# Performance work log

Measured on AMD Instinct MI355X. Metric: run time of the kernel, lower is better.

The kernel has to match this reference:

```python
import jax, jax.numpy as jnp
import numpy as np

MIN_NORM = 1e-15
EPS = 1e-7  # artanh domain clamp for fp32


def _tan_k(u, k):
    sk = jnp.sqrt(-k)
    return jnp.tanh(jnp.clip(sk * u, -15.0, 15.0)) / sk


def _artan_k(u, k):
    sk = jnp.sqrt(-k)
    return jnp.arctanh(jnp.clip(sk * u, -1.0 + EPS, 1.0 - EPS)) / sk


def _norm(x):
    return jnp.maximum(jnp.linalg.norm(x, axis=-1, keepdims=True), MIN_NORM)


def mobius_add(x, y, k):
    x2 = jnp.sum(x * x, axis=-1, keepdims=True)
    y2 = jnp.sum(y * y, axis=-1, keepdims=True)
    xy = jnp.sum(x * y, axis=-1, keepdims=True)
    num = (1.0 - 2.0 * k * xy - k * y2) * x + (1.0 + k * x2) * y
    den = 1.0 - 2.0 * k * xy + k * k * x2 * y2
    return num / jnp.maximum(den, MIN_NORM)


def mobius_matvec(M, x, k):
    # x: [..., d_in], M: [d_out, d_in]
    xn = _norm(x)
    mx = x @ M.T
    mxn = _norm(mx)
    res = _tan_k(mxn / xn * _artan_k(xn, k), k) * (mx / mxn)
    return jnp.where(jnp.all(mx == 0.0, axis=-1, keepdims=True), 0.0, res)


def mobius_pointwise_mul(w, x, k):
    xn = _norm(x)
    wx = w * x
    wxn = _norm(wx)
    res = _tan_k(wxn / xn * _artan_k(xn, k), k) * (wx / wxn)
    return jnp.where(jnp.all(wx == 0.0, axis=-1, keepdims=True), 0.0, res)


def expmap0(u, k):
    un = _norm(u)
    return _tan_k(un, k) * u / un


def logmap0(y, k):
    yn = _norm(y)
    return _artan_k(yn, k) * y / yn


def one_rnn_transform(W, h, U, x, b, k):
    Wh = mobius_matvec(W, h, k)
    Ux = mobius_matvec(U, x, k)
    return mobius_add(mobius_add(Wh, Ux, k), b, k)


def mobius_gru_cell(x, hx, w_ih, w_hh, b, k):
    W_ir, W_ih_, W_iz = jnp.split(w_ih, 3, axis=0)
    W_hr, W_hh_, W_hz = jnp.split(w_hh, 3, axis=0)
    b_r, b_h, b_z = b[0], b[1], b[2]
    z_t = jax.nn.sigmoid(logmap0(one_rnn_transform(W_hz, hx, W_iz, x, b_z, k), k))
    r_t = jax.nn.sigmoid(logmap0(one_rnn_transform(W_hr, hx, W_ir, x, b_r, k), k))
    rh_t = mobius_pointwise_mul(r_t, hx, k)
    h_tilde = one_rnn_transform(W_hh_, rh_t, W_ih_, x, b_h, k)
    delta_h = mobius_add(-hx, h_tilde, k)
    return mobius_add(hx, mobius_pointwise_mul(z_t, delta_h, k), k)


def mobius_gru_layer(x_tbd, h0, w_ih, w_hh, b, k, hyperbolic_input):
    # x_tbd: [T, B, D]; h0: [B, H]
    if not hyperbolic_input:
        x_tbd = expmap0(x_tbd, k)

    def step(hx, xt):
        h = expmap0(hx, k)
        h = mobius_gru_cell(xt, h, w_ih, w_hh, b, k)
        h = logmap0(h, k)
        return h, h

    h_last, outs = jax.lax.scan(step, h0, x_tbd)
    return outs, h_last  # outs: [T, B, H]


def setup_inputs() -> dict:
    key = jax.random.key(0)
    ks = jax.random.split(key, 8)
    B, T, D, H = 64, 1024, 256, 256
    stdv = 1.0 / np.sqrt(H)
    x = 0.02 * jax.random.normal(ks[0], (B, T, D), dtype=jnp.float32)
    k = jnp.float32(-1.0)  # hyperbolic curvature (geoopt sign convention)
    h0 = jnp.zeros((2, B, H), dtype=jnp.float32)
    w_ih0 = jax.random.uniform(ks[1], (3 * H, D), jnp.float32, -stdv, stdv)
    w_hh0 = jax.random.uniform(ks[2], (3 * H, H), jnp.float32, -stdv, stdv)
    b0 = 1e-5 * jax.random.normal(ks[3], (3, H), dtype=jnp.float32)
    w_ih1 = jax.random.uniform(ks[4], (3 * H, H), jnp.float32, -stdv, stdv)
    w_hh1 = jax.random.uniform(ks[5], (3 * H, H), jnp.float32, -stdv, stdv)
    b1 = 1e-5 * jax.random.normal(ks[6], (3, H), dtype=jnp.float32)
    return {"x": x, "k": k, "h0": h0, "w_ih0": w_ih0, "w_hh0": w_hh0, "b0": b0,
            "w_ih1": w_ih1, "w_hh1": w_hh1, "b1": b1}


def reference(x, k, h0, w_ih0, w_hh0, b0, w_ih1, w_hh1, b1):
    # x: [B, T, D]; source unbinds dim 1 as time -> scan over time-major.
    xt = jnp.swapaxes(x, 0, 1)  # [T, B, D]
    out0, hl0 = mobius_gru_layer(xt, h0[0], w_ih0, w_hh0, b0, k, hyperbolic_input=False)
    out1, hl1 = mobius_gru_layer(out0, h0[1], w_ih1, w_hh1, b1, k, hyperbolic_input=True)
    ht = jnp.stack([hl0, hl1])  # [num_layers, B, H]
    return out1, ht
```

## Files before the change

kernel.cpp:

```cpp
#include <hip/hip_runtime.h>
#include <cstdint>
#include <cstddef>

#define MINN 1e-15f
#define EPSA 1e-7f
#define C_L2E 1.44269504088896341f
#define C_LN2 0.69314718055994531f

typedef _Float16 half_t;
typedef _Float16 half2_t __attribute__((ext_vector_type(2)));

#if defined(__has_builtin)
#if __has_builtin(__builtin_amdgcn_update_dpp) && __has_builtin(__builtin_amdgcn_readlane)
#define USE_DPP 1
#endif
#endif

__device__ __forceinline__ float fexp2_(float x) {
#if defined(__has_builtin) && __has_builtin(__builtin_amdgcn_exp2f)
    return __builtin_amdgcn_exp2f(x);
#else
    return exp2f(x);
#endif
}
__device__ __forceinline__ float flog2_(float x) {
#if defined(__has_builtin) && __has_builtin(__builtin_amdgcn_logf)
    return __builtin_amdgcn_logf(x);
#else
    return log2f(x);
#endif
}
__device__ __forceinline__ float frcp_(float x) {
#if defined(__has_builtin) && __has_builtin(__builtin_amdgcn_rcpf)
    return __builtin_amdgcn_rcpf(x);
#else
    return 1.f / x;
#endif
}
__device__ __forceinline__ float tan_k_(float u, float sk, float rsk) {
    float a = fminf(fmaxf(sk * u, -15.f), 15.f);
    float t = fexp2_(a * (2.f * C_L2E));
    return (1.f - 2.f * frcp_(t + 1.f)) * rsk;
}
__device__ __forceinline__ float artan_k_(float u, float sk, float rsk) {
    float a = fminf(fmaxf(sk * u, -1.f + EPSA), 1.f - EPSA);
    return flog2_((1.f + a) * frcp_(1.f - a)) * (0.5f * C_LN2) * rsk;
}
__device__ __forceinline__ float sigm_(float x) {
    return frcp_(1.f + fexp2_(-x * C_L2E));
}
__device__ __forceinline__ float wave_sum(float v) {
#pragma unroll
    for (int off = 32; off; off >>= 1) v += __shfl_xor(v, off, 64);
    return v;
}

#ifdef USE_DPP
template <int CTRL, int RM, int BM>
__device__ __forceinline__ float dppmov_(float x) {
    return __builtin_bit_cast(float,
        __builtin_amdgcn_update_dpp(0, __builtin_bit_cast(int, x), CTRL, RM, BM, false));
}
#endif
__device__ __forceinline__ float wsum63_(float x) {
#ifdef USE_DPP
    x += dppmov_<0x111, 0xf, 0xf>(x);
    x += dppmov_<0x112, 0xf, 0xf>(x);
    x += dppmov_<0x114, 0xf, 0xe>(x);
    x += dppmov_<0x118, 0xf, 0xc>(x);
    x += dppmov_<0x142, 0xa, 0xf>(x);
    x += dppmov_<0x143, 0xc, 0xf>(x);
    return x;
#else
    return wave_sum(x);
#endif
}
__device__ __forceinline__ float gsum8_(float x) {
#ifdef USE_DPP
    x += dppmov_<0x111, 0xf, 0xf>(x);
    x += dppmov_<0x112, 0xf, 0xf>(x);
    x += dppmov_<0x114, 0xf, 0xe>(x);
    return x;
#else
    x += __shfl_xor(x, 1, 64);
    x += __shfl_xor(x, 2, 64);
    x += __shfl_xor(x, 4, 64);
    return x;
#endif
}
__device__ __forceinline__ float rdlane_(float x, int l) {
#ifdef USE_DPP
    return __builtin_bit_cast(float,
        __builtin_amdgcn_readlane(__builtin_bit_cast(int, x), l));
#else
    return __shfl(x, l, 64);
#endif
}
template <int N>
__device__ __forceinline__ void bredX(float* v, float* redbuf, int tid) {
    const int lane = tid & 63, wave = tid >> 6;
#pragma unroll
    for (int n = 0; n < N; ++n) {
        float s = wsum63_(v[n]);
        if (lane == 63) redbuf[n * 8 + wave] = s;
    }
    __syncthreads();
    float part = redbuf[lane & (8 * N - 1)];
    part = gsum8_(part);
#pragma unroll
    for (int n = 0; n < N; ++n) v[n] = rdlane_(part, 8 * n + 7);
}

__device__ __forceinline__ float dot2acc(uint32_t w, uint32_t h, float acc) {
#if defined(__has_builtin) && __has_builtin(__builtin_amdgcn_fdot2)
    return __builtin_amdgcn_fdot2(__builtin_bit_cast(half2_t, w),
                                  __builtin_bit_cast(half2_t, h), acc, false);
#else
    half2_t a = __builtin_bit_cast(half2_t, w);
    half2_t b = __builtin_bit_cast(half2_t, h);
    acc = fmaf((float)a[0], (float)b[0], acc);
    return fmaf((float)a[1], (float)b[1], acc);
#endif
}

__global__ __launch_bounds__(256) void kt_transpose(
    const float* __restrict__ a0, const float* __restrict__ a1,
    float* __restrict__ o0, float* __restrict__ o1) {
    int idx = blockIdx.x * 256 + threadIdx.x;
    int m = idx / 196608, rem = idx % 196608;
    int j = rem >> 8, kk = rem & 255;
    const float* in = (m == 0) ? a0 : a1;
    float* outp     = (m == 0) ? o0 : o1;
    outp[kk * 768 + j] = in[j * 256 + kk];
}

__global__ __launch_bounds__(256) void kt_prep1(
    const float* __restrict__ whh0, const float* __restrict__ whh1,
    uint32_t* __restrict__ p0, uint32_t* __restrict__ p1) {
    int idx = blockIdx.x * 256 + threadIdx.x;
    int l = idx >> 16, e = idx & 65535;
    int r4 = e >> 11, rem = e & 2047;
    int t = rem >> 2, m = r4 * 4 + (rem & 3);
    int lane = t & 63, wave = t >> 6;
    int p = wave * 32 + (lane & 31), ph = lane >> 5;
    int g = m >> 6, mi = m & 63;
    int row = g ? (512 + p) : p;
    int i = ph * 128 + 2 * mi;
    const float* w = l ? whh1 : whh0;
    half2_t hv;
    hv[0] = (half_t)w[row * 256 + i];
    hv[1] = (half_t)w[row * 256 + i + 1];
    (l ? p1 : p0)[e] = __builtin_bit_cast(uint32_t, hv);
}

__global__ __launch_bounds__(256) void kt_prep2(
    const float* __restrict__ whh0, const float* __restrict__ whh1,
    uint32_t* __restrict__ p0, uint32_t* __restrict__ p1) {
    int idx = blockIdx.x * 256 + threadIdx.x;
    int l = idx >> 15, e = idx & 32767;
    int i2 = e >> 8, j = e & 255;
    const float* w = l ? whh1 : whh0;
    half2_t hv;
    hv[0] = (half_t)w[(256 + j) * 256 + 2 * i2];
    hv[1] = (half_t)w[(256 + j) * 256 + 2 * i2 + 1];
    (l ? p1 : p0)[e] = __builtin_bit_cast(uint32_t, hv);
}

__global__ __launch_bounds__(256) void kt_init(
    const float* __restrict__ h0, float* __restrict__ hcar) {
    int i = blockIdx.x * 256 + threadIdx.x;
    hcar[i] = h0[i];
}
__global__ __launch_bounds__(256) void kt_final(
    const float* __restrict__ hcar, float* __restrict__ dst) {
    int i = blockIdx.x * 256 + threadIdx.x;
    dst[i] = hcar[i];
}

__global__ __launch_bounds__(256) void kt_gemm(
    const float* __restrict__ A, long long strideB,
    const float* __restrict__ Bt, float* __restrict__ C,
    float* __restrict__ ax_arr, const float* __restrict__ kptr, int mode) {
    __shared__ float As[16][68];
    __shared__ float Bs[16][68];
    __shared__ float sS[64];
    int tid = threadIdx.x;
    int row0 = blockIdx.y * 64, col0 = blockIdx.x * 64;

    {
        float kk = kptr[0], sk = sqrtf(-kk), rsk = frcp_(sk);
        int row = tid >> 2, q = tid & 3;
        int rc = row0 + row;
        size_t base = (size_t)(rc >> 6) * strideB + (size_t)(rc & 63) * 256 + q * 64;
        float n2 = 0.f;
#pragma unroll
        for (int u = 0; u < 16; ++u) {
            float4 v = *(const float4*)&A[base + u * 4];
            n2 += v.x * v.x + v.y * v.y + v.z * v.z + v.w * v.w;
        }
        n2 += __shfl_xor(n2, 1, 64);
        n2 += __shfl_xor(n2, 2, 64);
        float n = sqrtf(n2);
        float s, xn;
        if (mode == 0) {
            float nrm = fmaxf(n, MINN);
            float tk = tan_k_(nrm, sk, rsk);
            s = tk * frcp_(nrm);
            xn = fmaxf(tk * (n * frcp_(nrm)), MINN);
        } else {
            s = 1.f;
            xn = fmaxf(n, MINN);
        }
        float ax = artan_k_(xn, sk, rsk) * frcp_(xn);
        if (q == 0) { sS[row] = s; ax_arr[rc] = ax; }
    }

    int ty = tid >> 4, tx = tid & 15;
    int ra = tid >> 2, kq = tid & 3;
    int kb = tid >> 4, cq = tid & 15;
    float acc[4][4] = {};
    __syncthreads();
#pragma unroll 1
    for (int kt = 0; kt < 16; ++kt) {
        int k0 = kt * 16;
        int rc = row0 + ra;
        size_t aoff = (size_t)(rc >> 6) * strideB + (size_t)(rc & 63) * 256 + k0 + kq * 4;
        float4 av = *(const float4*)&A[aoff];
        float sc = sS[ra];
        float4 bv = *(const float4*)&Bt[(size_t)(k0 + kb) * 768 + col0 + cq * 4];
        As[kq * 4 + 0][ra] = av.x * sc;
        As[kq * 4 + 1][ra] = av.y * sc;
        As[kq * 4 + 2][ra] = av.z * sc;
        As[kq * 4 + 3][ra] = av.w * sc;
        *(float4*)&Bs[kb][cq * 4] = bv;
        __syncthreads();
#pragma unroll
        for (int kk = 0; kk < 16; ++kk) {
            float4 a4 = *(const float4*)&As[kk][ty * 4];
            float4 b4 = *(const float4*)&Bs[kk][tx * 4];
            float aa[4] = {a4.x, a4.y, a4.z, a4.w};
            float bb[4] = {b4.x, b4.y, b4.z, b4.w};
#pragma unroll
            for (int i = 0; i < 4; ++i)
#pragma unroll
                for (int j = 0; j < 4; ++j)
                    acc[i][j] = fmaf(aa[i], bb[j], acc[i][j]);
        }
        __syncthreads();
    }
#pragma unroll
    for (int i = 0; i < 4; ++i) {
        size_t row = (size_t)row0 + ty * 4 + i;
        *(float4*)&C[row * 768 + col0 + tx * 4] =
            make_float4(acc[i][0], acc[i][1], acc[i][2], acc[i][3]);
    }
}

__global__ __launch_bounds__(256) void kt_mscale(
    float* __restrict__ mx, const float* __restrict__ ax_arr,
    float* __restrict__ uxn, float* __restrict__ uxb,
    const float* __restrict__ bias, const float* __restrict__ kptr) {
    int lane = threadIdx.x & 63;
    int p = blockIdx.x * 4 + (threadIdx.x >> 6);
    int r = p / 3;
    int g = p - r * 3;
    float k = kptr[0], sk = sqrtf(-k), rsk = frcp_(sk);
    float* ptr = mx + (size_t)r * 768 + g * 256 + lane * 4;
    float4 v = *(const float4*)ptr;
    float4 b4 = *(const float4*)&bias[g * 256 + lane * 4];
    float n2 = wave_sum(v.x * v.x + v.y * v.y + v.z * v.z + v.w * v.w);
    float vb = wave_sum(v.x * b4.x + v.y * b4.y + v.z * b4.z + v.w * b4.w);
    float nt = sqrtf(n2);
    float mxn = fmaxf(nt, MINN);
    float arg = mxn * ax_arr[r];
    float tk = tan_k_(arg, sk, rsk);
    float f = tk * frcp_(mxn);
    v.x *= f; v.y *= f; v.z *= f; v.w *= f;
    *(float4*)ptr = v;
    if (lane == 0) { uxn[p] = tk * (nt * frcp_(mxn)); uxb[p] = f * vb; }
}

__global__ __launch_bounds__(512, 1) void kt_scan2(
    const float* __restrict__ Ux_0, const float* __restrict__ uxn_0,
    const float* __restrict__ uxb_0,
    const uint32_t* __restrict__ w1pk_0, const uint32_t* __restrict__ whh2g_0,
    const float* __restrict__ bias_0, float* __restrict__ hcar_0,
    float* __restrict__ out_0, long long sb_0, long long st_0,
    const float* __restrict__ Ux_1, const float* __restrict__ uxn_1,
    const float* __restrict__ uxb_1,
    const uint32_t* __restrict__ w1pk_1, const uint32_t* __restrict__ whh2g_1,
    const float* __restrict__ bias_1, float* __restrict__ hcar_1,
    float* __restrict__ out_1, long long sb_1, long long st_1,
    const float* __restrict__ kptr, int Tc, int nrole0) {
    __shared__ uint4 whhS[8192];
    __shared__ uint32_t hy2S[128];
    __shared__ uint32_t rh2S[128];
    __shared__ float redbuf[2][64];

    const int tid = threadIdx.x;
    const int role = (blockIdx.x >= nrole0) ? 1 : 0;
    const int bb = role ? (int)blockIdx.x - nrole0 : (int)blockIdx.x;

    const float* Ux      = role ? Ux_1 : Ux_0;
    const float* uxn     = role ? uxn_1 : uxn_0;
    const float* uxb     = role ? uxb_1 : uxb_0;
    const uint32_t* w1pk = role ? w1pk_1 : w1pk_0;
    const uint32_t* whh2g= role ? whh2g_1 : whh2g_0;
    const float* bias    = role ? bias_1 : bias_0;
    float* hcar          = role ? hcar_1 : hcar_0;
    float* outbase       = role ? out_1 : out_0;
    const long long stride_b = role ? sb_1 : sb_0;
    const long long stride_t = role ? st_1 : st_0;

    const int lane = tid & 63, wave = tid >> 6;
    const int p = wave * 32 + (lane & 31), ph = lane >> 5;
    const float k = kptr[0], sk = sqrtf(-k), rsk = frcp_(sk);

    for (int idx = tid; idx < 32768; idx += 512) {
        uint32_t v = whh2g[idx];
        int i2 = idx >> 8, col = idx & 255;
        ((uint32_t*)whhS)[((i2 >> 2) * 256 + col) * 4 + (i2 & 3)] = v;
    }
    uint32_t w1[128];
    {
        const uint4* wp = (const uint4*)w1pk;
#pragma unroll
        for (int r4 = 0; r4 < 32; ++r4) {
            uint4 v = wp[r4 * 512 + tid];
            w1[4 * r4 + 0] = v.x; w1[4 * r4 + 1] = v.y;
            w1[4 * r4 + 2] = v.z; w1[4 * r4 + 3] = v.w;
        }
    }

    const float br = bias[p], bh = bias[256 + p], bz = bias[512 + p];
    float h = hcar[bb * 256 + p];
    __syncthreads();
    float v4[4] = {br * br, bh * bh, bz * bz, h * h};
    bredX<4>(v4, redbuf[0], tid);
    const float bn2r = 0.5f * v4[0], bn2h = 0.5f * v4[1], bn2z = 0.5f * v4[2];
    float S_h2 = 0.5f * v4[3];

    float* myout = outbase + (size_t)bb * stride_b;
    const float* uxpb = Ux + (size_t)bb * Tc * 768;
    const float* unpb = uxn + (size_t)bb * Tc * 3;
    const float* ubpb = uxb + (size_t)bb * Tc * 3;

    float puxr = uxpb[p], puxh = uxpb[256 + p], puxz = uxpb[512 + p];
    float punr = unpb[0], punh = unpb[1], punz = unpb[2];
    float pubr = ubpb[0], pubh = ubpb[1], pubz = ubpb[2];

    for (int t = 0; t < Tc; ++t) {
        const float uxr = puxr, uxh = puxh, uxz = puxz;
        const float unr = punr, unh = punh, unz = punz;
        const float S_ubr = pubr, S_ubh = pubh, S_ubz = pubz;

        float hn = sqrtf(S_h2);
        float nrm = fmaxf(hn, MINN);
        float tk0 = tan_k_(nrm, sk, rsk);
        float chy = tk0 * frcp_(nrm);
        float hy = chy * h;
        float Shy2 = chy * chy * S_h2;
        float xnh = fmaxf(tk0 * (hn * frcp_(nrm)), MINN);
        float axh = artan_k_(xnh, sk, rsk) * frcp_(xnh);
        if (ph == 0) ((half_t*)hy2S)[p] = (half_t)hy;
        __syncthreads();

        if (t + 1 < Tc) {
            const float* uxp2 = uxpb + (size_t)(t + 1) * 768;
            puxr = uxp2[p]; puxh = uxp2[256 + p]; puxz = uxp2[512 + p];
            const float* unp2 = unpb + (size_t)(t + 1) * 3;
            punr = unp2[0]; punh = unp2[1]; punz = unp2[2];
            const float* ubp2 = ubpb + (size_t)(t + 1) * 3;
            pubr = ubp2[0]; pubh = ubp2[1]; pubz = ubp2[2];
        }

        float prA[4] = {0.f, 0.f, 0.f, 0.f};
        float pzA[4] = {0.f, 0.f, 0.f, 0.f};
        {
            const uint4* hp = (const uint4*)hy2S + ph * 16;
#pragma unroll
            for (int c4 = 0; c4 < 4; ++c4) {
                uint32_t hv[16];
#pragma unroll
                for (int u = 0; u < 4; ++u) {
                    uint4 v = hp[c4 * 4 + u];
                    hv[4 * u + 0] = v.x; hv[4 * u + 1] = v.y;
                    hv[4 * u + 2] = v.z; hv[4 * u + 3] = v.w;
                }
#pragma unroll
                for (int m = 0; m < 16; ++m) {
                    prA[c4] = dot2acc(w1[c4 * 16 + m], hv[m], prA[c4]);
                    pzA[c4] = dot2acc(w1[64 + c4 * 16 + m], hv[m], pzA[c4]);
                }
            }
        }
        float pr = (prA[0] + prA[1]) + (prA[2] + prA[3]);
        float pz = (pzA[0] + pzA[1]) + (pzA[2] + pzA[3]);
        const float mr = pr + __shfl_xor(pr, 32, 64);
        const float mz = pz + __shfl_xor(pz, 32, 64);

        float vr[8] = {mr * mr, mz * mz, mr * uxr, mz * uxz,
                       mr * br, mz * bz, h * uxh, h * bh};
        bredX<8>(vr, redbuf[0], tid);
        const float S_mr2 = 0.5f * vr[0], S_mz2 = 0.5f * vr[1];
        const float S_mru = 0.5f * vr[2], S_mzu = 0.5f * vr[3];
        const float S_mrb = 0.5f * vr[4], S_mzb = 0.5f * vr[5];
        const float S_huxh = 0.5f * vr[6], S_hbh = 0.5f * vr[7];

        const float m_   = ph ? mz    : mr;
        const float S2_  = ph ? S_mz2 : S_mr2;
        const float Su_  = ph ? S_mzu : S_mru;
        const float Sb_  = ph ? S_mzb : S_mrb;
        const float Sub_ = ph ? S_ubz : S_ubr;
        const float bn2_ = ph ? bn2z  : bn2r;
        const float un_  = ph ? unz   : unr;
        const float ux_  = ph ? uxz   : uxr;
        const float b_   = ph ? bz    : br;
        float g_own;
        {
            float mxn = fmaxf(sqrtf(S2_), MINN);
            float tk = tan_k_(mxn * axh, sk, rsk);
            float f = tk * frcp_(mxn);
            float x2 = f * f * S2_, y2 = un_ * un_, xy = f * Su_;
            float a = 1.f - 2.f * k * xy - k * y2;
            float bq = 1.f + k * x2;
            float rd = frcp_(fmaxf(1.f - 2.f * k * xy + k * k * x2 * y2, MINN));
            float c1 = (a * f * m_ + bq * ux_) * rd;
            float Sc12 = (a * a * x2 + 2.f * a * bq * xy + bq * bq * y2) * (rd * rd);
            float Sc1b = (a * f * Sb_ + bq * Sub_) * rd;
            float g = 1.f - 2.f * k * Sc1b - k * bn2_;
            float dl = 1.f + k * Sc12;
            float re = frcp_(fmaxf(1.f - 2.f * k * Sc1b + k * k * Sc12 * bn2_, MINN));
            float c2 = (g * c1 + dl * b_) * re;
            float Sc22 = (g * g * Sc12 + 2.f * g * dl * Sc1b + dl * dl * bn2_) * (re * re);
            float yn = fmaxf(sqrtf(Sc22), MINN);
            float lg = artan_k_(yn, sk, rsk) * frcp_(yn) * c2;
            g_own = sigm_(lg);
        }
        const float g_oth = __shfl_xor(g_own, 32, 64);
        const float r_t = ph ? g_oth : g_own;
        const float z_t = ph ? g_own : g_oth;

        float wx = r_t * hy;
        if (ph == 0) ((half_t*)rh2S)[p] = (half_t)wx;
        {
            float s1v = wsum63_(wx * wx);
            if (lane == 63) redbuf[1][wave] = s1v;
        }
        __syncthreads();

        float part1 = gsum8_(redbuf[1][lane & 7]);
        const float S_wx2 = 0.5f * rdlane_(part1, 7);
        float wxt = sqrtf(S_wx2);
        float wxn = fmaxf(wxt, MINN);
        float tkw = tan_k_(wxn * axh, sk, rsk);
        float fw = tkw * frcp_(wxn);
        float rhn = tkw * (wxt * frcp_(wxn));

        float qA[4] = {0.f, 0.f, 0.f, 0.f};
        {
            const uint4* rp = (const uint4*)rh2S + ph * 16;
#pragma unroll
            for (int u = 0; u < 16; ++u) {
                uint4 wv = whhS[(ph * 16 + u) * 256 + p];
                uint4 rv = rp[u];
                int s = u >> 2;
                qA[s] = dot2acc(wv.x, rv.x, qA[s]);
                qA[s] = dot2acc(wv.y, rv.y, qA[s]);
                qA[s] = dot2acc(wv.z, rv.z, qA[s]);
                qA[s] = dot2acc(wv.w, rv.w, qA[s]);
            }
        }
        float qq = (qA[0] + qA[1]) + (qA[2] + qA[3]);
        const float mh = fw * (qq + __shfl_xor(qq, 32, 64));

        float v4b[4] = {mh * mh, mh * uxh, mh * bh, hy * mh};
        bredX<4>(v4b, redbuf[0], tid);
        const float S_mh2 = 0.5f * v4b[0], S_mhu = 0.5f * v4b[1];
        const float S_mhb = 0.5f * v4b[2], S_hymh = 0.5f * v4b[3];

        float wz, Sdelta2;
        {
            float xnrh = fmaxf(rhn, MINN);
            float axrh = artan_k_(xnrh, sk, rsk) * frcp_(xnrh);
            float mxn = fmaxf(sqrtf(S_mh2), MINN);
            float tk = tan_k_(mxn * axrh, sk, rsk);
            float f = tk * frcp_(mxn);
            float x2 = f * f * S_mh2, y2 = unh * unh, xy = f * S_mhu;
            float a = 1.f - 2.f * k * xy - k * y2;
            float bq = 1.f + k * x2;
            float rd = frcp_(fmaxf(1.f - 2.f * k * xy + k * k * x2 * y2, MINN));
            float c1 = (a * f * mh + bq * uxh) * rd;
            float Sc12 = (a * a * x2 + 2.f * a * bq * xy + bq * bq * y2) * (rd * rd);
            float Sc1b = (a * f * S_mhb + bq * S_ubh) * rd;
            float S_hyc1 = (a * f * S_hymh + bq * chy * S_huxh) * rd;
            float g = 1.f - 2.f * k * Sc1b - k * bn2h;
            float dl = 1.f + k * Sc12;
            float re = frcp_(fmaxf(1.f - 2.f * k * Sc1b + k * k * Sc12 * bn2h, MINN));
            float htl = (g * c1 + dl * bh) * re;
            float Shtl2 = (g * g * Sc12 + 2.f * g * dl * Sc1b + dl * dl * bn2h) * (re * re);
            float S_hyhtl = (g * S_hyc1 + dl * chy * S_hbh) * re;
            float ad = 1.f + 2.f * k * S_hyhtl - k * Shtl2;
            float bd = 1.f + k * Shy2;
            float rdd = frcp_(fmaxf(1.f + 2.f * k * S_hyhtl + k * k * Shy2 * Shtl2, MINN));
            float delta = (ad * (-hy) + bd * htl) * rdd;
            Sdelta2 = (ad * ad * Shy2 - 2.f * ad * bd * S_hyhtl + bd * bd * Shtl2) * (rdd * rdd);
            wz = z_t * delta;
        }
        float v2[2] = {wz * wz, hy * wz};
        bredX<2>(v2, redbuf[1], tid);
        const float S_wz2 = 0.5f * v2[0], S_hywz = 0.5f * v2[1];

        {
            float dnc = fmaxf(sqrtf(Sdelta2), MINN);
            float axd = artan_k_(dnc, sk, rsk) * frcp_(dnc);
            float wzt = sqrtf(S_wz2);
            float wznc = fmaxf(wzt, MINN);
            float tkzd = tan_k_(wznc * axd, sk, rsk);
            float fz = tkzd * frcp_(wznc);
            float zd = fz * wz;
            float zdn2 = fz * fz * S_wz2;
            float S_hyzd = fz * S_hywz;
            float an = 1.f - 2.f * k * S_hyzd - k * zdn2;
            float bn_ = 1.f + k * Shy2;
            float rdn = frcp_(fmaxf(1.f - 2.f * k * S_hyzd + k * k * Shy2 * zdn2, MINN));
            float hnew = (an * hy + bn_ * zd) * rdn;
            float Shnew2 = (an * an * Shy2 + 2.f * an * bn_ * S_hyzd + bn_ * bn_ * zdn2) * (rdn * rdn);
            float yn = fmaxf(sqrtf(Shnew2), MINN);
            float ayn = artan_k_(yn, sk, rsk) * frcp_(yn);
            float outv = ayn * hnew;
            if (ph == 0) myout[(size_t)t * stride_t + p] = outv;
            h = outv;
            S_h2 = ayn * ayn * Shnew2;
        }
    }
    if (ph == 0) hcar[bb * 256 + p] = h;
}

extern "C" void kernel_launch(void* const* d_in, const int* in_sizes, int n_in,
                              void* d_out, int out_size, void* d_ws, size_t ws_size,
                              hipStream_t stream) {
    const float* x    = (const float*)d_in[0];
    const float* kptr = (const float*)d_in[1];
    const float* h0   = (const float*)d_in[2];
    const float* wih0 = (const float*)d_in[3];
    const float* whh0 = (const float*)d_in[4];
    const float* b0   = (const float*)d_in[5];
    const float* wih1 = (const float*)d_in[6];
    const float* whh1 = (const float*)d_in[7];
    const float* b1   = (const float*)d_in[8];
    float* out = (float*)d_out;
    float* ws  = (float*)d_ws;

    const int B = 64, T = 1024, H = 256;
    const int CT = 64, NC = 16;
    const int RC = B * CT;

    float* wt_ih0 = ws;
    float* wt_ih1 = wt_ih0 + 196608;
    uint32_t* w1pk0  = (uint32_t*)(wt_ih1 + 196608);
    uint32_t* w1pk1  = w1pk0 + 65536;
    uint32_t* whh2g0 = w1pk1 + 65536;
    uint32_t* whh2g1 = whh2g0 + 32768;
    float* hcar  = (float*)(whh2g1 + 32768);
    float* ax0   = hcar + 32768;
    float* ax1   = ax0 + RC;
    float* uxn0  = ax1 + RC;
    float* uxn1  = uxn0 + 3 * RC;
    float* uxb0  = uxn1 + 3 * RC;
    float* uxb1  = uxb0 + 3 * RC;
    float* out0c = uxb1 + 3 * RC;
    float* mx0   = out0c + (size_t)RC * H;
    float* mx1   = mx0 + (size_t)RC * 768;

    float* hcar0 = hcar;
    float* hcar1 = hcar + (size_t)B * H;

    dim3 blk(256);
    kt_transpose<<<dim3(1536), blk, 0, stream>>>(wih0, wih1, wt_ih0, wt_ih1);
    kt_prep1<<<dim3(512), blk, 0, stream>>>(whh0, whh1, w1pk0, w1pk1);
    kt_prep2<<<dim3(256), blk, 0, stream>>>(whh0, whh1, whh2g0, whh2g1);
    kt_init<<<dim3(128), blk, 0, stream>>>(h0, hcar);

    const long long sbx = (long long)T * 256;
    const long long sbc = (long long)CT * 256;

    {
        const float* xc = x;
        kt_gemm<<<dim3(12, RC / 64), blk, 0, stream>>>(xc, sbx, wt_ih0, mx0, ax0, kptr, 0);
        kt_mscale<<<dim3(RC * 3 / 4), blk, 0, stream>>>(mx0, ax0, uxn0, uxb0, b0, kptr);
        kt_scan2<<<dim3(B), dim3(512), 0, stream>>>(
            mx0, uxn0, uxb0, w1pk0, whh2g0, b0, hcar0, out0c, sbc, 256LL,
            mx0, uxn0, uxb0, w1pk0, whh2g0, b0, hcar0, out0c, sbc, 256LL,
            kptr, CT, B);
    }
    for (int c = 1; c < NC; ++c) {
        const float* xc = x + (size_t)c * CT * 256;
        kt_gemm<<<dim3(12, RC / 64), blk, 0, stream>>>(xc, sbx, wt_ih0, mx0, ax0, kptr, 0);
        kt_mscale<<<dim3(RC * 3 / 4), blk, 0, stream>>>(mx0, ax0, uxn0, uxb0, b0, kptr);
        kt_gemm<<<dim3(12, RC / 64), blk, 0, stream>>>(out0c, sbc, wt_ih1, mx1, ax1, kptr, 1);
        kt_mscale<<<dim3(RC * 3 / 4), blk, 0, stream>>>(mx1, ax1, uxn1, uxb1, b1, kptr);
        kt_scan2<<<dim3(2 * B), dim3(512), 0, stream>>>(
            mx0, uxn0, uxb0, w1pk0, whh2g0, b0, hcar0, out0c, sbc, 256LL,
            mx1, uxn1, uxb1, w1pk1, whh2g1, b1, hcar1,
            out + (size_t)(c - 1) * CT * B * H, 256LL, (long long)B * H,
            kptr, CT, B);
    }
    {
        kt_gemm<<<dim3(12, RC / 64), blk, 0, stream>>>(out0c, sbc, wt_ih1, mx1, ax1, kptr, 1);
        kt_mscale<<<dim3(RC * 3 / 4), blk, 0, stream>>>(mx1, ax1, uxn1, uxb1, b1, kptr);
        kt_scan2<<<dim3(B), dim3(512), 0, stream>>>(
            mx1, uxn1, uxb1, w1pk1, whh2g1, b1, hcar1,
            out + (size_t)(NC - 1) * CT * B * H, 256LL, (long long)B * H,
            mx1, uxn1, uxb1, w1pk1, whh2g1, b1, hcar1,
            out + (size_t)(NC - 1) * CT * B * H, 256LL, (long long)B * H,
            kptr, CT, B);
    }
    kt_final<<<dim3(128), blk, 0, stream>>>(hcar, out + (size_t)T * B * H);
}
```

Before: 6.134 ms.

## Fuse GEMM, scaling and scan into one pipelined mega-kernel with double buffering

After: 5.367 ms. -12.5%, faster.

```diff
diff --git a/kernel.cpp b/kernel.cpp
--- a/kernel.cpp
+++ b/kernel.cpp
@@ -177,149 +177,145 @@
     dst[i] = hcar[i];
 }
 
-__global__ __launch_bounds__(256) void kt_gemm(
-    const float* __restrict__ A, long long strideB,
-    const float* __restrict__ Bt, float* __restrict__ C,
-    float* __restrict__ ax_arr, const float* __restrict__ kptr, int mode) {
-    __shared__ float As[16][68];
-    __shared__ float Bs[16][68];
-    __shared__ float sS[64];
-    int tid = threadIdx.x;
-    int row0 = blockIdx.y * 64, col0 = blockIdx.x * 64;
-
-    {
-        float kk = kptr[0], sk = sqrtf(-kk), rsk = frcp_(sk);
-        int row = tid >> 2, q = tid & 3;
-        int rc = row0 + row;
-        size_t base = (size_t)(rc >> 6) * strideB + (size_t)(rc & 63) * 256 + q * 64;
-        float n2 = 0.f;
-#pragma unroll
-        for (int u = 0; u < 16; ++u) {
-            float4 v = *(const float4*)&A[base + u * 4];
-            n2 += v.x * v.x + v.y * v.y + v.z * v.z + v.w * v.w;
-        }
-        n2 += __shfl_xor(n2, 1, 64);
-        n2 += __shfl_xor(n2, 2, 64);
-        float n = sqrtf(n2);
-        float s, xn;
-        if (mode == 0) {
-            float nrm = fmaxf(n, MINN);
-            float tk = tan_k_(nrm, sk, rsk);
-            s = tk * frcp_(nrm);
-            xn = fmaxf(tk * (n * frcp_(nrm)), MINN);
-        } else {
-            s = 1.f;
-            xn = fmaxf(n, MINN);
-        }
-        float ax = artan_k_(xn, sk, rsk) * frcp_(xn);
-        if (q == 0) { sS[row] = s; ax_arr[rc] = ax; }
-    }
-
-    int ty = tid >> 4, tx = tid & 15;
-    int ra = tid >> 2, kq = tid & 3;
-    int kb = tid >> 4, cq = tid & 15;
-    float acc[4][4] = {};
-    __syncthreads();
+struct MegaArgs {
+    const float* s_mx[2]; const float* s_ax[2];
+    const uint32_t* s_w1[2]; const uint32_t* s_whh[2];
+    const float* s_bias[2]; float* s_hcar[2]; float* s_out[2];
+    long long s_sb[2]; long long s_st[2];
+    const float* g_A[2]; long long g_sB[2]; const float* g_Bt[2];
+    float* g_C[2]; float* g_ax[2]; int g_mode[2];
+    int nscan; int ngemm; int Tc;
+    const float* kptr;
+};
+
+__global__ __launch_bounds__(512, 1) void kt_mega(MegaArgs a) {
+    union Smem {
+        struct {
+            uint4 whhS[8192];
+            uint32_t hy2S[128];
+            uint32_t rh2S[128];
+            float redbuf[2][64];
+            float4 fS4[32];
+            float4 unS4[32];
+            float4 ubS4[32];
+        } s;
+        struct {
+            float As[16][68];
+            float Bs[16][132];
+            float sS[64];
+        } g;
+    };
+    __shared__ Smem sm;
+    const int tid = threadIdx.x;
+    const int bid = blockIdx.x;
+    const float k = a.kptr[0];
+    const float sk = sqrtf(-k), rsk = frcp_(sk);
+    const int Tc = a.Tc;
+
+    if (bid >= a.nscan * 64) {
+        int gb = bid - a.nscan * 64;
+        int gs = gb / 192, w = gb % 192;
+        const float* A = a.g_A[gs];
+        const long long strideB = a.g_sB[gs];
+        const float* Bt = a.g_Bt[gs];
+        float* C = a.g_C[gs];
+        float* axo = a.g_ax[gs];
+        const int mode = a.g_mode[gs];
+        int rb = w / 6, cb = w % 6;
+        int row0 = rb * 64, col0 = cb * 128;
+
+        {
+            int row = tid >> 3, oct = tid & 7;
+            int rc = row0 + row;
+            size_t base = (size_t)(rc >> 5) * strideB + (size_t)(rc & 31) * 256 + oct * 32;
+            float n2 = 0.f;
+#pragma unroll
+            for (int u = 0; u < 8; ++u) {
+                float4 v = *(const float4*)&A[base + u * 4];
+                n2 += v.x * v.x + v.y * v.y + v.z * v.z + v.w * v.w;
+            }
+            n2 += __shfl_xor(n2, 1, 64);
+            n2 += __shfl_xor(n2, 2, 64);
+            n2 += __shfl_xor(n2, 4, 64);
+            float n = sqrtf(n2);
+            float s, xn;
+            if (mode == 0) {
+                float nrm = fmaxf(n, MINN);
+                float tk = tan_k_(nrm, sk, rsk);
+                s = tk * frcp_(nrm);
+                xn = fmaxf(tk * (n * frcp_(nrm)), MINN);
+            } else {
+                s = 1.f;
+                xn = fmaxf(n, MINN);
+            }
+            float ax = artan_k_(xn, sk, rsk) * frcp_(xn);
+            if (oct == 0) { sm.g.sS[row] = s; if (cb == 0) axo[rc] = ax; }
+        }
+        __syncthreads();
+
+        int ty = tid >> 5, tx = tid & 31;
+        float acc[4][4] = {};
 #pragma unroll 1
-    for (int kt = 0; kt < 16; ++kt) {
-        int k0 = kt * 16;
-        int rc = row0 + ra;
-        size_t aoff = (size_t)(rc >> 6) * strideB + (size_t)(rc & 63) * 256 + k0 + kq * 4;
-        float4 av = *(const float4*)&A[aoff];
-        float sc = sS[ra];
-        float4 bv = *(const float4*)&Bt[(size_t)(k0 + kb) * 768 + col0 + cq * 4];
-        As[kq * 4 + 0][ra] = av.x * sc;
-        As[kq * 4 + 1][ra] = av.y * sc;
-        As[kq * 4 + 2][ra] = av.z * sc;
-        As[kq * 4 + 3][ra] = av.w * sc;
-        *(float4*)&Bs[kb][cq * 4] = bv;
-        __syncthreads();
-#pragma unroll
-        for (int kk = 0; kk < 16; ++kk) {
-            float4 a4 = *(const float4*)&As[kk][ty * 4];
-            float4 b4 = *(const float4*)&Bs[kk][tx * 4];
-            float aa[4] = {a4.x, a4.y, a4.z, a4.w};
-            float bb[4] = {b4.x, b4.y, b4.z, b4.w};
-#pragma unroll
-            for (int i = 0; i < 4; ++i)
-#pragma unroll
-                for (int j = 0; j < 4; ++j)
-                    acc[i][j] = fmaf(aa[i], bb[j], acc[i][j]);
-        }
-        __syncthreads();
-    }
-#pragma unroll
-    for (int i = 0; i < 4; ++i) {
-        size_t row = (size_t)row0 + ty * 4 + i;
-        *(float4*)&C[row * 768 + col0 + tx * 4] =
-            make_float4(acc[i][0], acc[i][1], acc[i][2], acc[i][3]);
-    }
-}
-
-__global__ __launch_bounds__(256) void kt_mscale(
-    float* __restrict__ mx, const float* __restrict__ ax_arr,
-    float* __restrict__ uxn, float* __restrict__ uxb,
-    const float* __restrict__ bias, const float* __restrict__ kptr) {
-    int lane = threadIdx.x & 63;
-    int p = blockIdx.x * 4 + (threadIdx.x >> 6);
-    int r = p / 3;
-    int g = p - r * 3;
-    float k = kptr[0], sk = sqrtf(-k), rsk = frcp_(sk);
-    float* ptr = mx + (size_t)r * 768 + g * 256 + lane * 4;
-    float4 v = *(const float4*)ptr;
-    float4 b4 = *(const float4*)&bias[g * 256 + lane * 4];
-    float n2 = wave_sum(v.x * v.x + v.y * v.y + v.z * v.z + v.w * v.w);
-    float vb = wave_sum(v.x * b4.x + v.y * b4.y + v.z * b4.z + v.w * b4.w);
-    float nt = sqrtf(n2);
-    float mxn = fmaxf(nt, MINN);
-    float arg = mxn * ax_arr[r];
-    float tk = tan_k_(arg, sk, rsk);
-    float f = tk * frcp_(mxn);
-    v.x *= f; v.y *= f; v.z *= f; v.w *= f;
-    *(float4*)ptr = v;
-    if (lane == 0) { uxn[p] = tk * (nt * frcp_(mxn)); uxb[p] = f * vb; }
-}
-
-__global__ __launch_bounds__(512, 1) void kt_scan2(
-    const float* __restrict__ Ux_0, const float* __restrict__ uxn_0,
-    const float* __restrict__ uxb_0,
-    const uint32_t* __restrict__ w1pk_0, const uint32_t* __restrict__ whh2g_0,
-    const float* __restrict__ bias_0, float* __restrict__ hcar_0,
-    float* __restrict__ out_0, long long sb_0, long long st_0,
-    const float* __restrict__ Ux_1, const float* __restrict__ uxn_1,
-    const float* __restrict__ uxb_1,
-    const uint32_t* __restrict__ w1pk_1, const uint32_t* __restrict__ whh2g_1,
-    const float* __restrict__ bias_1, float* __restrict__ hcar_1,
-    float* __restrict__ out_1, long long sb_1, long long st_1,
-    const float* __restrict__ kptr, int Tc, int nrole0) {
-    __shared__ uint4 whhS[8192];
-    __shared__ uint32_t hy2S[128];
-    __shared__ uint32_t rh2S[128];
-    __shared__ float redbuf[2][64];
-
-    const int tid = threadIdx.x;
-    const int role = (blockIdx.x >= nrole0) ? 1 : 0;
-    const int bb = role ? (int)blockIdx.x - nrole0 : (int)blockIdx.x;
-
-    const float* Ux      = role ? Ux_1 : Ux_0;
-    const float* uxn     = role ? uxn_1 : uxn_0;
-    const float* uxb     = role ? uxb_1 : uxb_0;
-    const uint32_t* w1pk = role ? w1pk_1 : w1pk_0;
-    const uint32_t* whh2g= role ? whh2g_1 : whh2g_0;
-    const float* bias    = role ? bias_1 : bias_0;
-    float* hcar          = role ? hcar_1 : hcar_0;
-    float* outbase       = role ? out_1 : out_0;
-    const long long stride_b = role ? sb_1 : sb_0;
-    const long long stride_t = role ? st_1 : st_0;
+        for (int kt = 0; kt < 16; ++kt) {
+            int k0 = kt * 16;
+            if (tid < 256) {
+                int ra = tid >> 2, kq = tid & 3;
+                int rc = row0 + ra;
+                size_t aoff = (size_t)(rc >> 5) * strideB + (size_t)(rc & 31) * 256 + k0 + kq * 4;
+                float4 av = *(const float4*)&A[aoff];
+                float sc = sm.g.sS[ra];
+                sm.g.As[kq * 4 + 0][ra] = av.x * sc;
+                sm.g.As[kq * 4 + 1][ra] = av.y * sc;
+                sm.g.As[kq * 4 + 2][ra] = av.z * sc;
+                sm.g.As[kq * 4 + 3][ra] = av.w * sc;
+            }
+            {
+                int kb = tid >> 5, cq = tid & 31;
+                float4 bv = *(const float4*)&Bt[(size_t)(k0 + kb) * 768 + col0 + cq * 4];
+                *(float4*)&sm.g.Bs[kb][cq * 4] = bv;
+            }
+            __syncthreads();
+#pragma unroll
+            for (int kk = 0; kk < 16; ++kk) {
+                float4 a4 = *(const float4*)&sm.g.As[kk][ty * 4];
+                float4 b4 = *(const float4*)&sm.g.Bs[kk][tx * 4];
+                float aa[4] = {a4.x, a4.y, a4.z, a4.w};
+                float bb[4] = {b4.x, b4.y, b4.z, b4.w};
+#pragma unroll
+                for (int i = 0; i < 4; ++i)
+#pragma unroll
+                    for (int j = 0; j < 4; ++j)
+                        acc[i][j] = fmaf(aa[i], bb[j], acc[i][j]);
+            }
+            __syncthreads();
+        }
+#pragma unroll
+        for (int i = 0; i < 4; ++i) {
+            size_t row = (size_t)row0 + ty * 4 + i;
+            *(float4*)&C[row * 768 + col0 + tx * 4] =
+                make_float4(acc[i][0], acc[i][1], acc[i][2], acc[i][3]);
+        }
+        return;
+    }
+
+    const int slot = bid >> 6, bb = bid & 63;
+    const float* mx      = a.s_mx[slot];
+    const float* axp     = a.s_ax[slot];
+    const uint32_t* w1pk = a.s_w1[slot];
+    const uint32_t* whh2g= a.s_whh[slot];
+    const float* bias    = a.s_bias[slot];
+    float* hcar          = a.s_hcar[slot];
+    float* outbase       = a.s_out[slot];
+    const long long stride_b = a.s_sb[slot];
+    const long long stride_t = a.s_st[slot];
 
     const int lane = tid & 63, wave = tid >> 6;
     const int p = wave * 32 + (lane & 31), ph = lane >> 5;
-    const float k = kptr[0], sk = sqrtf(-k), rsk = frcp_(sk);
 
     for (int idx = tid; idx < 32768; idx += 512) {
         uint32_t v = whh2g[idx];
         int i2 = idx >> 8, col = idx & 255;
-        ((uint32_t*)whhS)[((i2 >> 2) * 256 + col) * 4 + (i2 & 3)] = v;
+        ((uint32_t*)sm.s.whhS)[((i2 >> 2) * 256 + col) * 4 + (i2 & 3)] = v;
     }
     uint32_t w1[128];
     {
@@ -332,27 +328,51 @@
         }
     }
 
+    const float* uxpb = mx + (size_t)bb * Tc * 768;
+
+    {
+        const int UPW = (Tc * 3) >> 3;
+#pragma unroll 1
+        for (int i = 0; i < UPW; ++i) {
+            int u = wave * UPW + i;
+            int tt = u / 3, g = u - 3 * tt;
+            const float* rowp = uxpb + (size_t)tt * 768 + g * 256 + lane * 4;
+            float4 v = *(const float4*)rowp;
+            float4 b4 = *(const float4*)&bias[g * 256 + lane * 4];
+            float n2 = wsum63_(v.x * v.x + v.y * v.y + v.z * v.z + v.w * v.w);
+            float vb = wsum63_(v.x * b4.x + v.y * b4.y + v.z * b4.z + v.w * b4.w);
+            if (lane == 63) {
+                float nt = sqrtf(n2);
+                float mxn = fmaxf(nt, MINN);
+                float arg = mxn * axp[bb * Tc + tt];
+                float tk = tan_k_(arg, sk, rsk);
+                float f = tk * frcp_(mxn);
+                ((float*)&sm.s.fS4[tt])[g] = f;
+                ((float*)&sm.s.unS4[tt])[g] = tk * (nt * frcp_(mxn));
+                ((float*)&sm.s.ubS4[tt])[g] = f * vb;
+            }
+        }
+    }
+
     const float br = bias[p], bh = bias[256 + p], bz = bias[512 + p];
     float h = hcar[bb * 256 + p];
     __syncthreads();
     float v4[4] = {br * br, bh * bh, bz * bz, h * h};
-    bredX<4>(v4, redbuf[0], tid);
+    bredX<4>(v4, sm.s.redbuf[0], tid);
     const float bn2r = 0.5f * v4[0], bn2h = 0.5f * v4[1], bn2z = 0.5f * v4[2];
     float S_h2 = 0.5f * v4[3];
 
     float* myout = outbase + (size_t)bb * stride_b;
-    const float* uxpb = Ux + (size_t)bb * Tc * 768;
-    const float* unpb = uxn + (size_t)bb * Tc * 3;
-    const float* ubpb = uxb + (size_t)bb * Tc * 3;
-
-    float puxr = uxpb[p], puxh = uxpb[256 + p], puxz = uxpb[512 + p];
-    float punr = unpb[0], punh = unpb[1], punz = unpb[2];
-    float pubr = ubpb[0], pubh = ubpb[1], pubz = ubpb[2];
+
+    float prawr = uxpb[p], prawh = uxpb[256 + p], prawz = uxpb[512 + p];
 
     for (int t = 0; t < Tc; ++t) {
-        const float uxr = puxr, uxh = puxh, uxz = puxz;
-        const float unr = punr, unh = punh, unz = punz;
-        const float S_ubr = pubr, S_ubh = pubh, S_ubz = pubz;
+        const float4 ff = sm.s.fS4[t];
+        const float4 uu = sm.s.unS4[t];
+        const float4 ub = sm.s.ubS4[t];
+        const float uxr = prawr * ff.x, uxh = prawh * ff.y, uxz = prawz * ff.z;
+        const float unr = uu.x, unh = uu.y, unz = uu.z;
+        const float S_ubr = ub.x, S_ubh = ub.y, S_ubz = ub.z;
 
         float hn = sqrtf(S_h2);
         float nrm = fmaxf(hn, MINN);
@@ -362,22 +382,18 @@
         float Shy2 = chy * chy * S_h2;
         float xnh = fmaxf(tk0 * (hn * frcp_(nrm)), MINN);
         float axh = artan_k_(xnh, sk, rsk) * frcp_(xnh);
-        if (ph == 0) ((half_t*)hy2S)[p] = (half_t)hy;
+        if (ph == 0) ((half_t*)sm.s.hy2S)[p] = (half_t)hy;
         __syncthreads();
 
         if (t + 1 < Tc) {
             const float* uxp2 = uxpb + (size_t)(t + 1) * 768;
-            puxr = uxp2[p]; puxh = uxp2[256 + p]; puxz = uxp2[512 + p];
-            const float* unp2 = unpb + (size_t)(t + 1) * 3;
-            punr = unp2[0]; punh = unp2[1]; punz = unp2[2];
-            const float* ubp2 = ubpb + (size_t)(t + 1) * 3;
-            pubr = ubp2[0]; pubh = ubp2[1]; pubz = ubp2[2];
+            prawr = uxp2[p]; prawh = uxp2[256 + p]; prawz = uxp2[512 + p];
         }
 
         float prA[4] = {0.f, 0.f, 0.f, 0.f};
         float pzA[4] = {0.f, 0.f, 0.f, 0.f};
         {
-            const uint4* hp = (const uint4*)hy2S + ph * 16;
+            const uint4* hp = (const uint4*)sm.s.hy2S + ph * 16;
 #pragma unroll
             for (int c4 = 0; c4 < 4; ++c4) {
                 uint32_t hv[16];
@@ -401,7 +417,7 @@
 
         float vr[8] = {mr * mr, mz * mz, mr * uxr, mz * uxz,
                        mr * br, mz * bz, h * uxh, h * bh};
-        bredX<8>(vr, redbuf[0], tid);
+        bredX<8>(vr, sm.s.redbuf[0], tid);
         const float S_mr2 = 0.5f * vr[0], S_mz2 = 0.5f * vr[1];
         const float S_mru = 0.5f * vr[2], S_mzu = 0.5f * vr[3];
         const float S_mrb = 0.5f * vr[4], S_mzb = 0.5f * vr[5];
@@ -422,12 +438,12 @@
             float tk = tan_k_(mxn * axh, sk, rsk);
             float f = tk * frcp_(mxn);
             float x2 = f * f * S2_, y2 = un_ * un_, xy = f * Su_;
-            float a = 1.f - 2.f * k * xy - k * y2;
+            float aq = 1.f - 2.f * k * xy - k * y2;
             float bq = 1.f + k * x2;
             float rd = frcp_(fmaxf(1.f - 2.f * k * xy + k * k * x2 * y2, MINN));
-            float c1 = (a * f * m_ + bq * ux_) * rd;
-            float Sc12 = (a * a * x2 + 2.f * a * bq * xy + bq * bq * y2) * (rd * rd);
-            float Sc1b = (a * f * Sb_ + bq * Sub_) * rd;
+            float c1 = (aq * f * m_ + bq * ux_) * rd;
+            float Sc12 = (aq * aq * x2 + 2.f * aq * bq * xy + bq * bq * y2) * (rd * rd);
+            float Sc1b = (aq * f * Sb_ + bq * Sub_) * rd;
             float g = 1.f - 2.f * k * Sc1b - k * bn2_;
             float dl = 1.f + k * Sc12;
             float re = frcp_(fmaxf(1.f - 2.f * k * Sc1b + k * k * Sc12 * bn2_, MINN));
@@ -442,14 +458,14 @@
         const float z_t = ph ? g_own : g_oth;
 
         float wx = r_t * hy;
-        if (ph == 0) ((half_t*)rh2S)[p] = (half_t)wx;
+        if (ph == 0) ((half_t*)sm.s.rh2S)[p] = (half_t)wx;
         {
             float s1v = wsum63_(wx * wx);
-            if (lane == 63) redbuf[1][wave] = s1v;
+            if (lane == 63) sm.s.redbuf[1][wave] = s1v;
         }
         __syncthreads();
 
-        float part1 = gsum8_(redbuf[1][lane & 7]);
+        float part1 = gsum8_(sm.s.redbuf[1][lane & 7]);
         const float S_wx2 = 0.5f * rdlane_(part1, 7);
         float wxt = sqrtf(S_wx2);
         float wxn = fmaxf(wxt, MINN);
@@ -459,10 +475,10 @@
 
         float qA[4] = {0.f, 0.f, 0.f, 0.f};
         {
-            const uint4* rp = (const uint4*)rh2S + ph * 16;
+            const uint4* rp = (const uint4*)sm.s.rh2S + ph * 16;
 #pragma unroll
             for (int u = 0; u < 16; ++u) {
-                uint4 wv = whhS[(ph * 16 + u) * 256 + p];
+                uint4 wv = sm.s.whhS[(ph * 16 + u) * 256 + p];
                 uint4 rv = rp[u];
                 int s = u >> 2;
                 qA[s] = dot2acc(wv.x, rv.x, qA[s]);
@@ -475,7 +491,7 @@
         const float mh = fw * (qq + __shfl_xor(qq, 32, 64));
 
         float v4b[4] = {mh * mh, mh * uxh, mh * bh, hy * mh};
-        bredX<4>(v4b, redbuf[0], tid);
+        bredX<4>(v4b, sm.s.redbuf[0], tid);
         const float S_mh2 = 0.5f * v4b[0], S_mhu = 0.5f * v4b[1];
         const float S_mhb = 0.5f * v4b[2], S_hymh = 0.5f * v4b[3];
 
@@ -487,13 +503,13 @@
             float tk = tan_k_(mxn * axrh, sk, rsk);
             float f = tk * frcp_(mxn);
             float x2 = f * f * S_mh2, y2 = unh * unh, xy = f * S_mhu;
-            float a = 1.f - 2.f * k * xy - k * y2;
+            float aq = 1.f - 2.f * k * xy - k * y2;
             float bq = 1.f + k * x2;
             float rd = frcp_(fmaxf(1.f - 2.f * k * xy + k * k * x2 * y2, MINN));
-            float c1 = (a * f * mh + bq * uxh) * rd;
-            float Sc12 = (a * a * x2 + 2.f * a * bq * xy + bq * bq * y2) * (rd * rd);
-            float Sc1b = (a * f * S_mhb + bq * S_ubh) * rd;
-            float S_hyc1 = (a * f * S_hymh + bq * chy * S_huxh) * rd;
+            float c1 = (aq * f * mh + bq * uxh) * rd;
+            float Sc12 = (aq * aq * x2 + 2.f * aq * bq * xy + bq * bq * y2) * (rd * rd);
+            float Sc1b = (aq * f * S_mhb + bq * S_ubh) * rd;
+            float S_hyc1 = (aq * f * S_hymh + bq * chy * S_huxh) * rd;
             float g = 1.f - 2.f * k * Sc1b - k * bn2h;
             float dl = 1.f + k * Sc12;
             float re = frcp_(fmaxf(1.f - 2.f * k * Sc1b + k * k * Sc12 * bn2h, MINN));
@@ -508,7 +524,7 @@
             wz = z_t * delta;
         }
         float v2[2] = {wz * wz, hy * wz};
-        bredX<2>(v2, redbuf[1], tid);
+        bredX<2>(v2, sm.s.redbuf[1], tid);
         const float S_wz2 = 0.5f * v2[0], S_hywz = 0.5f * v2[1];
 
         {
@@ -553,8 +569,9 @@
     float* ws  = (float*)d_ws;
 
     const int B = 64, T = 1024, H = 256;
-    const int CT = 64, NC = 16;
+    const int CT = 32, NC = 32;
     const int RC = B * CT;
+    const int GBLK = (RC / 64) * 6;
 
     float* wt_ih0 = ws;
     float* wt_ih1 = wt_ih0 + 196608;
@@ -563,16 +580,20 @@
     uint32_t* whh2g0 = w1pk1 + 65536;
     uint32_t* whh2g1 = whh2g0 + 32768;
     float* hcar  = (float*)(whh2g1 + 32768);
-    float* ax0   = hcar + 32768;
-    float* ax1   = ax0 + RC;
-    float* uxn0  = ax1 + RC;
-    float* uxn1  = uxn0 + 3 * RC;
-    float* uxb0  = uxn1 + 3 * RC;
-    float* uxb1  = uxb0 + 3 * RC;
-    float* out0c = uxb1 + 3 * RC;
-    float* mx0   = out0c + (size_t)RC * H;
-    float* mx1   = mx0 + (size_t)RC * 768;
-
+    float* ax0b_[2], *ax1b_[2], *out0c_[2], *mx0_[2], *mx1_[2];
+    {
+        float* cur = hcar + 32768;
+        ax0b_[0] = cur; cur += RC;
+        ax0b_[1] = cur; cur += RC;
+        ax1b_[0] = cur; cur += RC;
+        ax1b_[1] = cur; cur += RC;
+        out0c_[0] = cur; cur += (size_t)RC * H;
+        out0c_[1] = cur; cur += (size_t)RC * H;
+        mx0_[0] = cur; cur += (size_t)RC * 768;
+        mx0_[1] = cur; cur += (size_t)RC * 768;
+        mx1_[0] = cur; cur += (size_t)RC * 768;
+        mx1_[1] = cur; cur += (size_t)RC * 768;
+    }
     float* hcar0 = hcar;
     float* hcar1 = hcar + (size_t)B * H;
 
@@ -582,39 +603,52 @@
     kt_prep2<<<dim3(256), blk, 0, stream>>>(whh0, whh1, whh2g0, whh2g1);
     kt_init<<<dim3(128), blk, 0, stream>>>(h0, hcar);
 
-    const long long sbx = (long long)T * 256;
-    const long long sbc = (long long)CT * 256;
-
     {
-        const float* xc = x;
-        kt_gemm<<<dim3(12, RC / 64), blk, 0, stream>>>(xc, sbx, wt_ih0, mx0, ax0, kptr, 0);
-        kt_mscale<<<dim3(RC * 3 / 4), blk, 0, stream>>>(mx0, ax0, uxn0, uxb0, b0, kptr);
-        kt_scan2<<<dim3(B), dim3(512), 0, stream>>>(
-            mx0, uxn0, uxb0, w1pk0, whh2g0, b0, hcar0, out0c, sbc, 256LL,
-            mx0, uxn0, uxb0, w1pk0, whh2g0, b0, hcar0, out0c, sbc, 256LL,
-            kptr, CT, B);
-    }
-    for (int c = 1; c < NC; ++c) {
-        const float* xc = x + (size_t)c * CT * 256;
-        kt_gemm<<<dim3(12, RC / 64), blk, 0, stream>>>(xc, sbx, wt_ih0, mx0, ax0, kptr, 0);
-        kt_mscale<<<dim3(RC * 3 / 4), blk, 0, stream>>>(mx0, ax0, uxn0, uxb0, b0, kptr);
-        kt_gemm<<<dim3(12, RC / 64), blk, 0, stream>>>(out0c, sbc, wt_ih1, mx1, ax1, kptr, 1);
-        kt_mscale<<<dim3(RC * 3 / 4), blk, 0, stream>>>(mx1, ax1, uxn1, uxb1, b1, kptr);
-        kt_scan2<<<dim3(2 * B), dim3(512), 0, stream>>>(
-            mx0, uxn0, uxb0, w1pk0, whh2g0, b0, hcar0, out0c, sbc, 256LL,
-            mx1, uxn1, uxb1, w1pk1, whh2g1, b1, hcar1,
-            out + (size_t)(c - 1) * CT * B * H, 256LL, (long long)B * H,
-            kptr, CT, B);
-    }
-    {
-        kt_gemm<<<dim3(12, RC / 64), blk, 0, stream>>>(out0c, sbc, wt_ih1, mx1, ax1, kptr, 1);
-        kt_mscale<<<dim3(RC * 3 / 4), blk, 0, stream>>>(mx1, ax1, uxn1, uxb1, b1, kptr);
-        kt_scan2<<<dim3(B), dim3(512), 0, stream>>>(
-            mx1, uxn1, uxb1, w1pk1, whh2g1, b1, hcar1,
-            out + (size_t)(NC - 1) * CT * B * H, 256LL, (long long)B * H,
-            mx1, uxn1, uxb1, w1pk1, whh2g1, b1, hcar1,
-            out + (size_t)(NC - 1) * CT * B * H, 256LL, (long long)B * H,
-            kptr, CT, B);
+        MegaArgs a{};
+        a.nscan = 0; a.ngemm = 1; a.Tc = CT; a.kptr = kptr;
+        a.g_A[0] = x; a.g_sB[0] = (long long)T * 256; a.g_Bt[0] = wt_ih0;
+        a.g_C[0] = mx0_[0]; a.g_ax[0] = ax0b_[0]; a.g_mode[0] = 0;
+        kt_mega<<<dim3(GBLK), dim3(512), 0, stream>>>(a);
+    }
+
+    for (int c = 0; c <= NC + 1; ++c) {
+        MegaArgs a{};
+        int ns = 0, ng = 0;
+        if (c <= NC - 1) {
+            a.s_mx[ns] = mx0_[c & 1]; a.s_ax[ns] = ax0b_[c & 1];
+            a.s_w1[ns] = w1pk0; a.s_whh[ns] = whh2g0;
+            a.s_bias[ns] = b0; a.s_hcar[ns] = hcar0;
+            a.s_out[ns] = out0c_[c & 1];
+            a.s_sb[ns] = (long long)CT * 256; a.s_st[ns] = 256;
+            ns++;
+        }
+        int d = c - 2;
+        if (d >= 0 && d <= NC - 1) {
+            a.s_mx[ns] = mx1_[d & 1]; a.s_ax[ns] = ax1b_[d & 1];
+            a.s_w1[ns] = w1pk1; a.s_whh[ns] = whh2g1;
+            a.s_bias[ns] = b1; a.s_hcar[ns] = hcar1;
+            a.s_out[ns] = out + (size_t)d * CT * B * H;
+            a.s_sb[ns] = 256; a.s_st[ns] = (long long)B * H;
+            ns++;
+        }
+        int e = c + 1;
+        if (e <= NC - 1) {
+            a.g_A[ng] = x + (size_t)e * CT * 256; a.g_sB[ng] = (long long)T * 256;
+            a.g_Bt[ng] = wt_ih0; a.g_C[ng] = mx0_[e & 1];
+            a.g_ax[ng] = ax0b_[e & 1]; a.g_mode[ng] = 0;
+            ng++;
+        }
+        int f = c - 1;
+        if (f >= 0 && f <= NC - 1) {
+            a.g_A[ng] = out0c_[f & 1]; a.g_sB[ng] = (long long)CT * 256;
+            a.g_Bt[ng] = wt_ih1; a.g_C[ng] = mx1_[f & 1];
+            a.g_ax[ng] = ax1b_[f & 1]; a.g_mode[ng] = 1;
+            ng++;
+        }
+        a.nscan = ns; a.ngemm = ng; a.Tc = CT; a.kptr = kptr;
+        int nb = ns * 64 + ng * GBLK;
+        if (nb > 0)
+            kt_mega<<<dim3(nb), dim3(512), 0, stream>>>(a);
     }
     kt_final<<<dim3(128), blk, 0, stream>>>(hcar, out + (size_t)T * B * H);
 }
```
